# Kernel optimization log

Measured on AMD Instinct MI355X. Metric: run time of the kernel, lower is better.

The kernel has to match this reference:

```python
import jax, jax.numpy as jnp
import numpy as np

NUM_CLASSES = 3
CLASSES_WEIGHT = np.array([1.0, 1.0, 1.0], dtype=np.float32)


def setup_inputs() -> dict:
    key = jax.random.key(0)
    k1, k2 = jax.random.split(key)
    B = 8192
    s = jax.random.normal(k1, (B, NUM_CLASSES), dtype=jnp.float32)
    t = jax.random.randint(k2, (B,), 0, NUM_CLASSES, dtype=jnp.int64)
    return {"s": s, "t": t}


def reference(s, t):
    B, C = s.shape
    # new_target = clamp(one_hot(t), 1e-4, 1.0) * classes_weight
    T = jnp.clip(jax.nn.one_hot(t, C, dtype=s.dtype), 0.0001, 1.0)
    T = T * jnp.asarray(CLASSES_WEIGHT, dtype=s.dtype)
    # new_source = softmax(s); we need log(new_source) and log(new_target)
    logS = jax.nn.log_softmax(s, axis=1)  # [B, C]
    logT = jnp.log(T)                      # [B, C]
    # a_ij = -sum_c T[j]*(logS[i]-logT[j]); b_ij = -sum_c T[j]*(logT[i]-logT[j])
    # a_ij - b_ij = sum_c T[j,c] * (logT[i,c] - logS[i,c])
    D = logT - logS                        # [B, C]
    M = jnp.einsum('ic,jc->ij', D, T)      # [B, B] pairwise matrix
    loss = 0.0001 + jnp.sum(jnp.abs(M)) / (B * B)
    return loss
```

## Files before the change

kernel.cpp:

```cpp
#include <hip/hip_runtime.h>

#define NCLS 3
#define BLOCK 1024
#define NWAVES (BLOCK / 64)

__global__ __launch_bounds__(BLOCK) void self_l2_kernel(
    const float* __restrict__ s, const int* __restrict__ t,
    float* __restrict__ out, int B) {
  constexpr float EPS = 1e-4f;
  constexpr float LOG_EPS = -9.210340371976182f;
  constexpr float OME = 1.0f - EPS;

  double a0 = 0.0, a1 = 0.0, a2 = 0.0;
  double c0 = 0.0, c1 = 0.0, c2 = 0.0;

  for (int i = threadIdx.x; i < B; i += BLOCK) {
    const float s0 = s[3 * i + 0];
    const float s1 = s[3 * i + 1];
    const float s2 = s[3 * i + 2];
    const int ti = t[i];

    const float m = fmaxf(s0, fmaxf(s1, s2));
    const float lse = m + logf(expf(s0 - m) + expf(s1 - m) + expf(s2 - m));
    const float ls0 = s0 - lse, ls1 = s1 - lse, ls2 = s2 - lse;

    const float lt0 = (ti == 0) ? 0.0f : LOG_EPS;
    const float lt1 = (ti == 1) ? 0.0f : LOG_EPS;
    const float lt2 = (ti == 2) ? 0.0f : LOG_EPS;

    const float D0 = lt0 - ls0, D1 = lt1 - ls1, D2 = lt2 - ls2;
    const float sD = D0 + D1 + D2;

    a0 += (double)fabsf(EPS * sD + OME * D0);
    a1 += (double)fabsf(EPS * sD + OME * D1);
    a2 += (double)fabsf(EPS * sD + OME * D2);
    c0 += (ti == 0) ? 1.0 : 0.0;
    c1 += (ti == 1) ? 1.0 : 0.0;
    c2 += (ti == 2) ? 1.0 : 0.0;
  }

  for (int off = 32; off > 0; off >>= 1) {
    a0 += __shfl_down(a0, off);
    a1 += __shfl_down(a1, off);
    a2 += __shfl_down(a2, off);
    c0 += __shfl_down(c0, off);
    c1 += __shfl_down(c1, off);
    c2 += __shfl_down(c2, off);
  }

  __shared__ double sm[NWAVES][6];
  const int lane = threadIdx.x & 63;
  const int wave = threadIdx.x >> 6;
  if (lane == 0) {
    sm[wave][0] = a0; sm[wave][1] = a1; sm[wave][2] = a2;
    sm[wave][3] = c0; sm[wave][4] = c1; sm[wave][5] = c2;
  }
  __syncthreads();

  if (threadIdx.x == 0) {
    double A0 = 0, A1 = 0, A2 = 0, C0 = 0, C1 = 0, C2 = 0;
    for (int w = 0; w < NWAVES; ++w) {
      A0 += sm[w][0]; A1 += sm[w][1]; A2 += sm[w][2];
      C0 += sm[w][3]; C1 += sm[w][4]; C2 += sm[w][5];
    }
    const double Bd = (double)B;
    const double loss = 1e-4 + (C0 * A0 + C1 * A1 + C2 * A2) / (Bd * Bd);
    out[0] = (float)loss;
  }
}

extern "C" void kernel_launch(void* const* d_in, const int* in_sizes, int n_in,
                              void* d_out, int out_size, void* d_ws, size_t ws_size,
                              hipStream_t stream) {
  const float* s = (const float*)d_in[0];
  const int* t = (const int*)d_in[1];
  float* out = (float*)d_out;
  const int B = in_sizes[0] / NCLS;
  self_l2_kernel<<<dim3(1), dim3(BLOCK), 0, stream>>>(s, t, out, B);
}
```

Before: 60.91 us.

## Split reduction into multi-block partial pass plus finalize kernel with vectorized loads

Replaces the single 1024-thread block with a grid of 64-thread blocks that each handle four rows per thread using float4/int4 loads. Each block writes six double partials to workspace, and a second single-wave kernel sums them and computes the loss. The aim is to spread the memory traffic and the exp/log math across many CUs instead of one. The cost is a second kernel launch and a round trip through global memory for the partials.

```diff
diff --git a/kernel.cpp b/kernel.cpp
--- a/kernel.cpp
+++ b/kernel.cpp
@@ -1,42 +1,58 @@
 #include <hip/hip_runtime.h>
 
 #define NCLS 3
-#define BLOCK 1024
-#define NWAVES (BLOCK / 64)
+#define K1_BLOCK 64
 
-__global__ __launch_bounds__(BLOCK) void self_l2_kernel(
-    const float* __restrict__ s, const int* __restrict__ t,
-    float* __restrict__ out, int B) {
+__device__ __forceinline__ void accum_row(float s0, float s1, float s2, int ti,
+                                          double& a0, double& a1, double& a2,
+                                          double& c0, double& c1, double& c2) {
   constexpr float EPS = 1e-4f;
   constexpr float LOG_EPS = -9.210340371976182f;
   constexpr float OME = 1.0f - EPS;
 
-  double a0 = 0.0, a1 = 0.0, a2 = 0.0;
-  double c0 = 0.0, c1 = 0.0, c2 = 0.0;
+  const float m = fmaxf(s0, fmaxf(s1, s2));
+  const float lse = m + logf(expf(s0 - m) + expf(s1 - m) + expf(s2 - m));
+  const float ls0 = s0 - lse, ls1 = s1 - lse, ls2 = s2 - lse;
 
-  for (int i = threadIdx.x; i < B; i += BLOCK) {
-    const float s0 = s[3 * i + 0];
-    const float s1 = s[3 * i + 1];
-    const float s2 = s[3 * i + 2];
-    const int ti = t[i];
+  const float lt0 = (ti == 0) ? 0.0f : LOG_EPS;
+  const float lt1 = (ti == 1) ? 0.0f : LOG_EPS;
+  const float lt2 = (ti == 2) ? 0.0f : LOG_EPS;
 
-    const float m = fmaxf(s0, fmaxf(s1, s2));
-    const float lse = m + logf(expf(s0 - m) + expf(s1 - m) + expf(s2 - m));
-    const float ls0 = s0 - lse, ls1 = s1 - lse, ls2 = s2 - lse;
+  const float D0 = lt0 - ls0, D1 = lt1 - ls1, D2 = lt2 - ls2;
+  const float sD = D0 + D1 + D2;
 
-    const float lt0 = (ti == 0) ? 0.0f : LOG_EPS;
-    const float lt1 = (ti == 1) ? 0.0f : LOG_EPS;
-    const float lt2 = (ti == 2) ? 0.0f : LOG_EPS;
+  a0 += (double)fabsf(EPS * sD + OME * D0);
+  a1 += (double)fabsf(EPS * sD + OME * D1);
+  a2 += (double)fabsf(EPS * sD + OME * D2);
+  c0 += (ti == 0) ? 1.0 : 0.0;
+  c1 += (ti == 1) ? 1.0 : 0.0;
+  c2 += (ti == 2) ? 1.0 : 0.0;
+}
 
-    const float D0 = lt0 - ls0, D1 = lt1 - ls1, D2 = lt2 - ls2;
-    const float sD = D0 + D1 + D2;
+__global__ __launch_bounds__(K1_BLOCK) void partial_kernel(
+    const float* __restrict__ s, const int* __restrict__ t,
+    double* __restrict__ ws, int B) {
+  const int quanta = B >> 2;
+  const int gtid = blockIdx.x * K1_BLOCK + threadIdx.x;
+  const int gstride = gridDim.x * K1_BLOCK;
 
-    a0 += (double)fabsf(EPS * sD + OME * D0);
-    a1 += (double)fabsf(EPS * sD + OME * D1);
-    a2 += (double)fabsf(EPS * sD + OME * D2);
-    c0 += (ti == 0) ? 1.0 : 0.0;
-    c1 += (ti == 1) ? 1.0 : 0.0;
-    c2 += (ti == 2) ? 1.0 : 0.0;
+  double a0 = 0, a1 = 0, a2 = 0, c0 = 0, c1 = 0, c2 = 0;
+
+  for (int j = gtid; j < quanta; j += gstride) {
+    const float4 f0 = ((const float4*)s)[3 * j + 0];
+    const float4 f1 = ((const float4*)s)[3 * j + 1];
+    const float4 f2 = ((const float4*)s)[3 * j + 2];
+    const int4 tv = ((const int4*)t)[j];
+
+    accum_row(f0.x, f0.y, f0.z, tv.x, a0, a1, a2, c0, c1, c2);
+    accum_row(f0.w, f1.x, f1.y, tv.y, a0, a1, a2, c0, c1, c2);
+    accum_row(f1.z, f1.w, f2.x, tv.z, a0, a1, a2, c0, c1, c2);
+    accum_row(f2.y, f2.z, f2.w, tv.w, a0, a1, a2, c0, c1, c2);
+  }
+
+  if (gtid == 0) {
+    for (int i = quanta << 2; i < B; ++i)
+      accum_row(s[3 * i], s[3 * i + 1], s[3 * i + 2], t[i], a0, a1, a2, c0, c1, c2);
   }
 
   for (int off = 32; off > 0; off >>= 1) {
@@ -48,24 +64,30 @@
     c2 += __shfl_down(c2, off);
   }
 
-  __shared__ double sm[NWAVES][6];
-  const int lane = threadIdx.x & 63;
-  const int wave = threadIdx.x >> 6;
-  if (lane == 0) {
-    sm[wave][0] = a0; sm[wave][1] = a1; sm[wave][2] = a2;
-    sm[wave][3] = c0; sm[wave][4] = c1; sm[wave][5] = c2;
+  if (threadIdx.x == 0) {
+    double* p = ws + (size_t)blockIdx.x * 6;
+    p[0] = a0; p[1] = a1; p[2] = a2;
+    p[3] = c0; p[4] = c1; p[5] = c2;
   }
-  __syncthreads();
+}
 
-  if (threadIdx.x == 0) {
-    double A0 = 0, A1 = 0, A2 = 0, C0 = 0, C1 = 0, C2 = 0;
-    for (int w = 0; w < NWAVES; ++w) {
-      A0 += sm[w][0]; A1 += sm[w][1]; A2 += sm[w][2];
-      C0 += sm[w][3]; C1 += sm[w][4]; C2 += sm[w][5];
-    }
+__global__ __launch_bounds__(64) void finalize_kernel(
+    const double* __restrict__ ws, float* __restrict__ out, int B, int nb) {
+  const int l = threadIdx.x;
+  const int c = l >> 3;
+  const int b0 = l & 7;
+  double v = 0.0;
+  if (c < 6) {
+    for (int b = b0; b < nb; b += 8) v += ws[b * 6 + c];
+  }
+  v += __shfl_down(v, 4, 8);
+  v += __shfl_down(v, 2, 8);
+  v += __shfl_down(v, 1, 8);
+  const double A0 = __shfl(v, 0),  A1 = __shfl(v, 8),  A2 = __shfl(v, 16);
+  const double C0 = __shfl(v, 24), C1 = __shfl(v, 32), C2 = __shfl(v, 40);
+  if (l == 0) {
     const double Bd = (double)B;
-    const double loss = 1e-4 + (C0 * A0 + C1 * A1 + C2 * A2) / (Bd * Bd);
-    out[0] = (float)loss;
+    out[0] = (float)(1e-4 + (C0 * A0 + C1 * A1 + C2 * A2) / (Bd * Bd));
   }
 }
 
@@ -75,6 +97,14 @@
   const float* s = (const float*)d_in[0];
   const int* t = (const int*)d_in[1];
   float* out = (float*)d_out;
+  double* ws = (double*)d_ws;
   const int B = in_sizes[0] / NCLS;
-  self_l2_kernel<<<dim3(1), dim3(BLOCK), 0, stream>>>(s, t, out, B);
+
+  const int quanta = B >> 2;
+  int nb = (quanta + K1_BLOCK - 1) / K1_BLOCK;
+  if (nb < 1) nb = 1;
+  if (nb > 256) nb = 256;
+
+  partial_kernel<<<dim3(nb), dim3(K1_BLOCK), 0, stream>>>(s, t, ws, B);
+  finalize_kernel<<<dim3(1), dim3(64), 0, stream>>>(ws, out, B, nb);
 }
```

Result: faster. 57.24 us (-6.0%).
